# Kernel tuning notes

Hardware: AMD Instinct MI355X
Metric: run time of the kernel (lower is better)

## Reference

```python
import jax, jax.numpy as jnp
import numpy as np

C1, CS = 512, 32
EPS = 1e-5
_HI, _HJ = np.triu_indices(CS, k=1)  # pairwise (i<j) hadamard index pairs, cs_expand = 496


def setup_inputs() -> dict:
    key = jax.random.key(0)
    ks = jax.random.split(key, 9)
    B, H, W = 16, 32, 32
    return dict(
        x=jax.random.normal(ks[0], (B, C1, H, W), jnp.float32),
        fc_w=jax.random.normal(ks[1], (C1, C1), jnp.float32) * 0.05,   # 1x1 conv kernel
        fc_b=jax.random.normal(ks[2], (C1,), jnp.float32) * 0.05,
        bn_gamma=jax.random.normal(ks[3], (C1,), jnp.float32) * 0.1 + 1.0,
        bn_beta=jax.random.normal(ks[4], (C1,), jnp.float32) * 0.1,
        bn_mean=jax.random.normal(ks[5], (C1,), jnp.float32) * 0.1,    # BN running mean
        bn_var=jax.random.uniform(ks[6], (C1,), jnp.float32) + 0.5,    # BN running var (positive)
        eva_w=jax.random.normal(ks[7], (C1, C1), jnp.float32) * 0.05,
        eva_b=jax.random.normal(ks[8], (C1,), jnp.float32) * 0.05,
    )


def reference(x, fc_w, fc_b, bn_gamma, bn_beta, bn_mean, bn_var, eva_w, eva_b):
    hi = jnp.asarray(_HI)
    hj = jnp.asarray(_HJ)
    # 1x1 conv (pointwise GEMM over channels)
    x = jnp.einsum('bchw,oc->bohw', x, fc_w) + fc_b[None, :, None, None]
    # BatchNorm2d, eval mode (running stats)
    scale = bn_gamma / jnp.sqrt(bn_var + EPS)
    x = (x - bn_mean[None, :, None, None]) * scale[None, :, None, None] + bn_beta[None, :, None, None]
    # channel evaluation logits: global avg pool -> linear
    logits = jnp.mean(x, axis=(2, 3)) @ eva_w.T + eva_b  # [B, C1]
    # top-cs channel selection and gather (eval path)
    _, idx = jax.lax.top_k(logits, CS)                    # [B, CS]
    x_sel = jax.vmap(lambda xi, ii: xi[ii])(x, idx)       # [B, CS, H, W]
    # pairwise hadamard expansion: gather-multiply over (i<j) pairs
    prod = x_sel[:, hi] * x_sel[:, hj]                    # [B, cs_expand, H, W]
    # CrossHadaNorm: per-channel standardize with batch stats, affine from
    # cross-products of norm_x affine params gathered via hadamard_i/j
    mean = jnp.mean(prod, axis=(0, 2, 3), keepdims=True)
    var = jnp.var(prod, axis=(0, 2, 3), keepdims=True)
    g = (bn_gamma[hi] * bn_gamma[hj])[None, :, None, None]
    b = (bn_beta[hi] * bn_beta[hj])[None, :, None, None]
    prod = (prod - mean) / jnp.sqrt(var + EPS) * g + b
    return jnp.concatenate([x, prod], axis=1)             # [B, c1 + cs_expand, H, W]
```

## Files before the change

### kernel.cpp

```cpp
#include <hip/hip_runtime.h>
#include <stdint.h>
#include <stddef.h>

#define B_   16
#define C1_  512
#define HW_  1024
#define CS_  32
#define CE_  496
#define CO_  1008

typedef __attribute__((ext_vector_type(8))) short short8;
typedef __attribute__((ext_vector_type(4))) short short4v;
typedef __attribute__((ext_vector_type(4))) float f32x4;

__device__ __forceinline__ short f2bf(float f) {
  unsigned u = __builtin_bit_cast(unsigned, f);
  unsigned r = (u + 0x7fffu + ((u >> 16) & 1u)) >> 16;
  return (short)(unsigned short)r;
}

__device__ __forceinline__ void gload_lds16(const void* g, void* l) {
  __builtin_amdgcn_global_load_lds(
      (const __attribute__((address_space(1))) unsigned int*)g,
      (__attribute__((address_space(3))) unsigned int*)l, 16, 0, 0);
}

__global__ __launch_bounds__(256) void transpose_pool(const float* __restrict__ x,
                                                      short* __restrict__ xT,
                                                      float* __restrict__ partial,
                                                      const float* __restrict__ fc_w,
                                                      const float* __restrict__ fc_b,
                                                      const float* __restrict__ bn_gamma,
                                                      const float* __restrict__ bn_beta,
                                                      const float* __restrict__ bn_mean,
                                                      const float* __restrict__ bn_var,
                                                      short* __restrict__ wbf,
                                                      float* __restrict__ bs,
                                                      float* __restrict__ bb) {
  int bid = blockIdx.x;
  int tid = threadIdx.x;
  if (bid >= 2048) {
    if (bid < 3072) {
      int i = (bid - 2048) * 256 + tid;
      wbf[i] = f2bf(fc_w[i]);
    } else {
      for (int o = tid; o < C1_; o += 256) {
        float s = bn_gamma[o] / sqrtf(bn_var[o] + 1e-5f);
        bs[o] = s;
        bb[o] = (fc_b[o] - bn_mean[o]) * s + bn_beta[o];
      }
    }
    return;
  }
  __shared__ float tile[64][65];
  int b = bid >> 7;
  int tt = bid & 127;
  int ct = tt >> 4, pt = tt & 15;
  int c0 = ct * 64, p0 = pt * 64;
  int rr = tid >> 4, lc = tid & 15;
  const float* xb = x + (size_t)b * C1_ * HW_;
#pragma unroll
  for (int it = 0; it < 4; ++it) {
    int c = it * 16 + rr;
    int p4 = lc * 4;
    float4 v = *(const float4*)(xb + (size_t)(c0 + c) * HW_ + p0 + p4);
    tile[c][p4+0] = v.x; tile[c][p4+1] = v.y; tile[c][p4+2] = v.z; tile[c][p4+3] = v.w;
    float g = v.x + v.y + v.z + v.w;
    g += __shfl_down(g, 8, 16);
    g += __shfl_down(g, 4, 16);
    g += __shfl_down(g, 2, 16);
    g += __shfl_down(g, 1, 16);
    if (lc == 0) partial[((size_t)b * 16 + pt) * C1_ + c0 + c] = g;
  }
  __syncthreads();
#pragma unroll
  for (int it = 0; it < 4; ++it) {
    int p = it * 16 + rr;
    int c4 = lc * 4;
    short4v o;
    o[0] = f2bf(tile[c4+0][p]);
    o[1] = f2bf(tile[c4+1][p]);
    o[2] = f2bf(tile[c4+2][p]);
    o[3] = f2bf(tile[c4+3][p]);
    *(short4v*)(xT + (size_t)b * HW_ * C1_ + (size_t)(p0 + p) * C1_ + c0 + c4) = o;
  }
}

__global__ __launch_bounds__(64) void fc_pool_kernel(
    const float* __restrict__ partial, const float* __restrict__ fc_w,
    const float* __restrict__ bs, const float* __restrict__ bb,
    float* __restrict__ pb) {
  int b = blockIdx.x >> 3, ot = blockIdx.x & 7;
  int tid = threadIdx.x;
  __shared__ float px[512];
  for (int c = tid; c < 512; c += 64) {
    float s = 0.f;
#pragma unroll
    for (int pt = 0; pt < 16; ++pt) s += partial[((size_t)b * 16 + pt) * C1_ + c];
    px[c] = s * (1.f / 1024.f);
  }
  __syncthreads();
  int o = ot * 64 + tid;
  const float4* wr = (const float4*)(fc_w + (size_t)o * 512);
  float acc = 0.f;
#pragma unroll 8
  for (int q = 0; q < 128; ++q) {
    float4 w = wr[q];
    acc += w.x * px[q*4] + w.y * px[q*4+1] + w.z * px[q*4+2] + w.w * px[q*4+3];
  }
  pb[b * 512 + o] = acc * bs[o] + bb[o];
}

__global__ __launch_bounds__(64) void eva_kernel(
    const float* __restrict__ pb, const float* __restrict__ eva_w,
    const float* __restrict__ eva_b, float* __restrict__ logits) {
  int b = blockIdx.x >> 3, ot = blockIdx.x & 7;
  int tid = threadIdx.x;
  __shared__ float ps[512];
  for (int c = tid; c < 512; c += 64) ps[c] = pb[b * 512 + c];
  __syncthreads();
  int o = ot * 64 + tid;
  const float4* wr = (const float4*)(eva_w + (size_t)o * 512);
  float acc = 0.f;
#pragma unroll 8
  for (int q = 0; q < 128; ++q) {
    float4 w = wr[q];
    acc += w.x * ps[q*4] + w.y * ps[q*4+1] + w.z * ps[q*4+2] + w.w * ps[q*4+3];
  }
  logits[b * 512 + o] = acc + eva_b[o];
}

__global__ __launch_bounds__(64) void topk_kernel(const float* __restrict__ logits,
                                                  int* __restrict__ idx) {
  int b = blockIdx.x, lane = threadIdx.x;
  float v[8];
  int base = lane * 8;
#pragma unroll
  for (int u = 0; u < 8; ++u) v[u] = logits[b * 512 + base + u];
  for (int it = 0; it < CS_; ++it) {
    float bv = v[0]; int bu = 0;
#pragma unroll
    for (int u = 1; u < 8; ++u) if (v[u] > bv) { bv = v[u]; bu = u; }
    int bi = base + bu;
    for (int off = 32; off; off >>= 1) {
      float ov = __shfl_down(bv, off);
      int   oi = __shfl_down(bi, off);
      if (ov > bv || (ov == bv && oi < bi)) { bv = ov; bi = oi; }
    }
    bi = __shfl(bi, 0);
    if (lane == 0) idx[b * CS_ + it] = bi;
#pragma unroll
    for (int u = 0; u < 8; ++u) if (bi == base + u) v[u] = -3.4e38f;
  }
}

__global__ __launch_bounds__(256) void gemm_kernel(const short* __restrict__ W,
                                                   const short* __restrict__ XT,
                                                   const float* __restrict__ bs,
                                                   const float* __restrict__ bb,
                                                   float* __restrict__ out) {
  __shared__ char smem[65536];
  int bid = (blockIdx.x & 7) * 64 + (blockIdx.x >> 3);
  int b = bid >> 5;
  int t = bid & 31;
  int mt = t & 3, ntile = t >> 2;
  int m0 = mt * 128, n0 = ntile * 128;
  const short* Ag = W + (size_t)m0 * 512;
  const short* Bg = XT + (size_t)b * HW_ * 512 + (size_t)n0 * 512;
  int tid = threadIdx.x;
  int lane = tid & 63, wave = tid >> 6;
  int wr = wave >> 1, wc = wave & 1;
  int mrow = wr * 64, ncol = wc * 64;
  int lrow = lane & 15;
  int swz = (lrow & 7) << 4;

  f32x4 acc[4][4];
#pragma unroll
  for (int i = 0; i < 4; ++i)
#pragma unroll
    for (int j = 0; j < 4; ++j) acc[i][j] = (f32x4){0.f, 0.f, 0.f, 0.f};

#define STAGE(dstbase, k0)                                                      \
  {                                                                             \
    _Pragma("unroll")                                                           \
    for (int it_ = 0; it_ < 4; ++it_) {                                         \
      int s_ = it_ * 256 + tid;                                                 \
      int L_ = s_ * 16;                                                         \
      int row_ = L_ >> 7;                                                       \
      int w_ = L_ & 127;                                                        \
      int srcs_ = (w_ ^ ((row_ & 7) << 4)) >> 1;                                \
      gload_lds16(Ag + (size_t)row_ * 512 + (k0) + srcs_,                       \
                  smem + (dstbase) + L_);                                       \
      gload_lds16(Bg + (size_t)row_ * 512 + (k0) + srcs_,                       \
                  smem + 32768 + (dstbase) + L_);                               \
    }                                                                           \
  }

  STAGE(0, 0)
  asm volatile("s_waitcnt vmcnt(0)" ::: "memory");
  __syncthreads();

  int cur = 0;
  for (int kt = 0; kt < 8; ++kt) {
    if (kt < 7) STAGE((cur ^ 1) * 16384, (kt + 1) * 64)
    const char* Ab = smem + cur * 16384;
    const char* Bb = smem + 32768 + cur * 16384;
#pragma unroll
    for (int kk = 0; kk < 2; ++kk) {
      int kb = (kk * 64 + (lane >> 4) * 16) ^ swz;
      short8 af[4], bfv[4];
#pragma unroll
      for (int f = 0; f < 4; ++f) {
        af[f]  = *(const short8*)(Ab + (mrow + f * 16 + lrow) * 128 + kb);
        bfv[f] = *(const short8*)(Bb + (ncol + f * 16 + lrow) * 128 + kb);
      }
#pragma unroll
      for (int mf = 0; mf < 4; ++mf)
#pragma unroll
        for (int nf = 0; nf < 4; ++nf)
          acc[mf][nf] = __builtin_amdgcn_mfma_f32_16x16x32_bf16(af[mf], bfv[nf], acc[mf][nf], 0, 0, 0);
    }
    asm volatile("s_waitcnt vmcnt(0)" ::: "memory");
    __syncthreads();
    cur ^= 1;
  }

  float* outb = out + (size_t)b * CO_ * HW_;
#pragma unroll
  for (int mf = 0; mf < 4; ++mf) {
#pragma unroll
    for (int j = 0; j < 4; ++j) {
      int o = m0 + mrow + mf * 16 + (lane >> 4) * 4 + j;
      float s = bs[o], bv = bb[o];
#pragma unroll
      for (int nf = 0; nf < 4; ++nf) {
        int p = n0 + ncol + nf * 16 + lrow;
        outb[(size_t)o * HW_ + p] = acc[mf][nf][j] * s + bv;
      }
    }
  }
#undef STAGE
}

__global__ __launch_bounds__(256) void hada_kernel(
    const int* __restrict__ idx, const float* __restrict__ bn_gamma,
    const float* __restrict__ bn_beta, float* __restrict__ out) {
  int e = blockIdx.x, tid = threadIdx.x;
  int lane = tid & 63, wave = tid >> 6;
  int i = 0, rem = e;
  while (rem >= 31 - i) { rem -= 31 - i; ++i; }
  int j = i + 1 + rem;

  __shared__ int chi[16], chj[16];
  if (tid < 16) chi[tid] = idx[tid * CS_ + i];
  else if (tid < 32) chj[tid - 16] = idx[(tid - 16) * CS_ + j];
  __syncthreads();

  f32x4 p[16];
  float s = 0.f, s2 = 0.f;
#pragma unroll
  for (int b = 0; b < 16; ++b) {
    const float4* xi = (const float4*)(out + ((size_t)b * CO_ + chi[b]) * HW_);
    const float4* xj = (const float4*)(out + ((size_t)b * CO_ + chj[b]) * HW_);
    float4 a = xi[tid], c = xj[tid];
    p[b][0] = a.x * c.x; p[b][1] = a.y * c.y; p[b][2] = a.z * c.z; p[b][3] = a.w * c.w;
    s  += p[b][0] + p[b][1] + p[b][2] + p[b][3];
    s2 += p[b][0]*p[b][0] + p[b][1]*p[b][1] + p[b][2]*p[b][2] + p[b][3]*p[b][3];
  }
  for (int off = 32; off; off >>= 1) { s += __shfl_down(s, off); s2 += __shfl_down(s2, off); }
  __shared__ float red[8];
  if (lane == 0) { red[wave] = s; red[4 + wave] = s2; }
  __syncthreads();
  float S  = red[0] + red[1] + red[2] + red[3];
  float S2 = red[4] + red[5] + red[6] + red[7];
  float mean = S * (1.f / 16384.f);
  float var  = S2 * (1.f / 16384.f) - mean * mean;
  float sc = (bn_gamma[i] * bn_gamma[j]) / sqrtf(var + 1e-5f);
  float bi_ = bn_beta[i] * bn_beta[j] - mean * sc;

#pragma unroll
  for (int b = 0; b < 16; ++b) {
    float4 r;
    r.x = p[b][0] * sc + bi_;
    r.y = p[b][1] * sc + bi_;
    r.z = p[b][2] * sc + bi_;
    r.w = p[b][3] * sc + bi_;
    ((float4*)(out + ((size_t)b * CO_ + C1_ + e) * HW_))[tid] = r;
  }
}

#define XT_OFF     ((size_t)0)
#define WBF_OFF    ((size_t)16777216)
#define PART_OFF   ((size_t)17301504)
#define PB_OFF     ((size_t)17825792)
#define LOG_OFF    ((size_t)17858560)
#define IDX_OFF    ((size_t)17891328)
#define BS_OFF     ((size_t)17893376)
#define BB_OFF     ((size_t)17895424)

extern "C" void kernel_launch(void* const* d_in, const int* in_sizes, int n_in,
                              void* d_out, int out_size, void* d_ws, size_t ws_size,
                              hipStream_t stream) {
  const float* x        = (const float*)d_in[0];
  const float* fc_w     = (const float*)d_in[1];
  const float* fc_b     = (const float*)d_in[2];
  const float* bn_gamma = (const float*)d_in[3];
  const float* bn_beta  = (const float*)d_in[4];
  const float* bn_mean  = (const float*)d_in[5];
  const float* bn_var   = (const float*)d_in[6];
  const float* eva_w    = (const float*)d_in[7];
  const float* eva_b    = (const float*)d_in[8];
  float* out = (float*)d_out;
  char* ws = (char*)d_ws;

  short* xT      = (short*)(ws + XT_OFF);
  short* wbf     = (short*)(ws + WBF_OFF);
  float* partial = (float*)(ws + PART_OFF);
  float* pb      = (float*)(ws + PB_OFF);
  float* logits  = (float*)(ws + LOG_OFF);
  int*   idx     = (int*)(ws + IDX_OFF);
  float* bs      = (float*)(ws + BS_OFF);
  float* bb      = (float*)(ws + BB_OFF);

  hipLaunchKernelGGL(transpose_pool, dim3(3073), dim3(256), 0, stream,
                     x, xT, partial, fc_w, fc_b, bn_gamma, bn_beta, bn_mean, bn_var,
                     wbf, bs, bb);
  hipLaunchKernelGGL(fc_pool_kernel, dim3(128), dim3(64), 0, stream,
                     partial, fc_w, bs, bb, pb);
  hipLaunchKernelGGL(eva_kernel, dim3(128), dim3(64), 0, stream,
                     pb, eva_w, eva_b, logits);
  hipLaunchKernelGGL(topk_kernel, dim3(16), dim3(64), 0, stream, logits, idx);
  hipLaunchKernelGGL(gemm_kernel, dim3(512), dim3(256), 0, stream, wbf, xT, bs, bb, out);
  hipLaunchKernelGGL(hada_kernel, dim3(CE_), dim3(256), 0, stream,
                     idx, bn_gamma, bn_beta, out);
}
```

Measured before the change: 90.11 us.

## Fuse pooled-FC into GEMM launch and deepen GEMM K pipeline to four stages

The small fc_pool computation now runs in 128 extra blocks appended to the GEMM grid, which removes one kernel launch and lets it overlap with the main GEMM. The GEMM main loop changes from a double-buffered 64-wide K tile to a four-buffer, 32-wide K tile pipeline with three loads in flight. It uses partial vmcnt waits and a new XOR swizzle for the 64-byte rows. This aims to hide global-to-LDS latency better, at the cost of more barriers per K step and extra code in the GEMM kernel.

```diff
diff --git a/kernel.cpp b/kernel.cpp
--- a/kernel.cpp
+++ b/kernel.cpp
@@ -86,31 +86,6 @@
   }
 }
 
-__global__ __launch_bounds__(64) void fc_pool_kernel(
-    const float* __restrict__ partial, const float* __restrict__ fc_w,
-    const float* __restrict__ bs, const float* __restrict__ bb,
-    float* __restrict__ pb) {
-  int b = blockIdx.x >> 3, ot = blockIdx.x & 7;
-  int tid = threadIdx.x;
-  __shared__ float px[512];
-  for (int c = tid; c < 512; c += 64) {
-    float s = 0.f;
-#pragma unroll
-    for (int pt = 0; pt < 16; ++pt) s += partial[((size_t)b * 16 + pt) * C1_ + c];
-    px[c] = s * (1.f / 1024.f);
-  }
-  __syncthreads();
-  int o = ot * 64 + tid;
-  const float4* wr = (const float4*)(fc_w + (size_t)o * 512);
-  float acc = 0.f;
-#pragma unroll 8
-  for (int q = 0; q < 128; ++q) {
-    float4 w = wr[q];
-    acc += w.x * px[q*4] + w.y * px[q*4+1] + w.z * px[q*4+2] + w.w * px[q*4+3];
-  }
-  pb[b * 512 + o] = acc * bs[o] + bb[o];
-}
-
 __global__ __launch_bounds__(64) void eva_kernel(
     const float* __restrict__ pb, const float* __restrict__ eva_w,
     const float* __restrict__ eva_b, float* __restrict__ logits) {
@@ -158,8 +133,38 @@
                                                    const short* __restrict__ XT,
                                                    const float* __restrict__ bs,
                                                    const float* __restrict__ bb,
-                                                   float* __restrict__ out) {
+                                                   float* __restrict__ out,
+                                                   const float* __restrict__ partial,
+                                                   const float* __restrict__ fc_w,
+                                                   float* __restrict__ pb) {
   __shared__ char smem[65536];
+  int tid = threadIdx.x;
+
+  if (blockIdx.x >= 512) {
+    int bid2 = blockIdx.x - 512;
+    int b = bid2 >> 3, ot = bid2 & 7;
+    float* px = (float*)smem;
+    for (int c = tid; c < 512; c += 256) {
+      float s = 0.f;
+#pragma unroll
+      for (int pt = 0; pt < 16; ++pt) s += partial[((size_t)b * 16 + pt) * C1_ + c];
+      px[c] = s * (1.f / 1024.f);
+    }
+    __syncthreads();
+    if (tid < 64) {
+      int o = ot * 64 + tid;
+      const float4* wr = (const float4*)(fc_w + (size_t)o * 512);
+      float acc = 0.f;
+#pragma unroll 8
+      for (int q = 0; q < 128; ++q) {
+        float4 w = wr[q];
+        acc += w.x * px[q*4] + w.y * px[q*4+1] + w.z * px[q*4+2] + w.w * px[q*4+3];
+      }
+      pb[b * 512 + o] = acc * bs[o] + bb[o];
+    }
+    return;
+  }
+
   int bid = (blockIdx.x & 7) * 64 + (blockIdx.x >> 3);
   int b = bid >> 5;
   int t = bid & 31;
@@ -167,12 +172,11 @@
   int m0 = mt * 128, n0 = ntile * 128;
   const short* Ag = W + (size_t)m0 * 512;
   const short* Bg = XT + (size_t)b * HW_ * 512 + (size_t)n0 * 512;
-  int tid = threadIdx.x;
   int lane = tid & 63, wave = tid >> 6;
   int wr = wave >> 1, wc = wave & 1;
   int mrow = wr * 64, ncol = wc * 64;
   int lrow = lane & 15;
-  int swz = (lrow & 7) << 4;
+  int slot = lane >> 4;
 
   f32x4 acc[4][4];
 #pragma unroll
@@ -180,50 +184,52 @@
 #pragma unroll
     for (int j = 0; j < 4; ++j) acc[i][j] = (f32x4){0.f, 0.f, 0.f, 0.f};
 
-#define STAGE(dstbase, k0)                                                      \
+#define STAGE(bufidx, k0)                                                       \
   {                                                                             \
     _Pragma("unroll")                                                           \
-    for (int it_ = 0; it_ < 4; ++it_) {                                         \
+    for (int it_ = 0; it_ < 2; ++it_) {                                         \
       int s_ = it_ * 256 + tid;                                                 \
       int L_ = s_ * 16;                                                         \
-      int row_ = L_ >> 7;                                                       \
-      int w_ = L_ & 127;                                                        \
-      int srcs_ = (w_ ^ ((row_ & 7) << 4)) >> 1;                                \
-      gload_lds16(Ag + (size_t)row_ * 512 + (k0) + srcs_,                       \
-                  smem + (dstbase) + L_);                                       \
-      gload_lds16(Bg + (size_t)row_ * 512 + (k0) + srcs_,                       \
-                  smem + 32768 + (dstbase) + L_);                               \
+      int row_ = L_ >> 6;                                                       \
+      int srcb_ = (L_ & 63) ^ (((row_ >> 1) & 3) << 4);                         \
+      gload_lds16(Ag + (size_t)row_ * 512 + (k0) + (srcb_ >> 1),                \
+                  smem + (bufidx) * 8192 + L_);                                 \
+      gload_lds16(Bg + (size_t)row_ * 512 + (k0) + (srcb_ >> 1),                \
+                  smem + 32768 + (bufidx) * 8192 + L_);                         \
     }                                                                           \
   }
 
+#define STEP(KT, VN)                                                            \
+  {                                                                             \
+    asm volatile("s_waitcnt vmcnt(" #VN ")" ::: "memory");                      \
+    __builtin_amdgcn_s_barrier();                                               \
+    if ((KT) + 3 < 16) STAGE(((KT) + 3) & 3, ((KT) + 3) * 32)                   \
+    const char* Ab = smem + ((KT) & 3) * 8192;                                  \
+    const char* Bb = smem + 32768 + ((KT) & 3) * 8192;                          \
+    short8 af[4], bfv[4];                                                       \
+    _Pragma("unroll")                                                           \
+    for (int f = 0; f < 4; ++f) {                                               \
+      int rowA = mrow + f * 16 + lrow;                                          \
+      af[f] = *(const short8*)(Ab + rowA * 64 + (slot ^ ((rowA >> 1) & 3)) * 16);\
+      int rowB = ncol + f * 16 + lrow;                                          \
+      bfv[f] = *(const short8*)(Bb + rowB * 64 + (slot ^ ((rowB >> 1) & 3)) * 16);\
+    }                                                                           \
+    _Pragma("unroll")                                                           \
+    for (int mf = 0; mf < 4; ++mf)                                              \
+      _Pragma("unroll")                                                         \
+      for (int nf = 0; nf < 4; ++nf)                                            \
+        acc[mf][nf] = __builtin_amdgcn_mfma_f32_16x16x32_bf16(af[mf], bfv[nf],  \
+                                                              acc[mf][nf], 0, 0, 0); \
+  }
+
   STAGE(0, 0)
-  asm volatile("s_waitcnt vmcnt(0)" ::: "memory");
-  __syncthreads();
-
-  int cur = 0;
-  for (int kt = 0; kt < 8; ++kt) {
-    if (kt < 7) STAGE((cur ^ 1) * 16384, (kt + 1) * 64)
-    const char* Ab = smem + cur * 16384;
-    const char* Bb = smem + 32768 + cur * 16384;
-#pragma unroll
-    for (int kk = 0; kk < 2; ++kk) {
-      int kb = (kk * 64 + (lane >> 4) * 16) ^ swz;
-      short8 af[4], bfv[4];
-#pragma unroll
-      for (int f = 0; f < 4; ++f) {
-        af[f]  = *(const short8*)(Ab + (mrow + f * 16 + lrow) * 128 + kb);
-        bfv[f] = *(const short8*)(Bb + (ncol + f * 16 + lrow) * 128 + kb);
-      }
-#pragma unroll
-      for (int mf = 0; mf < 4; ++mf)
-#pragma unroll
-        for (int nf = 0; nf < 4; ++nf)
-          acc[mf][nf] = __builtin_amdgcn_mfma_f32_16x16x32_bf16(af[mf], bfv[nf], acc[mf][nf], 0, 0, 0);
-    }
-    asm volatile("s_waitcnt vmcnt(0)" ::: "memory");
-    __syncthreads();
-    cur ^= 1;
-  }
+  STAGE(1, 32)
+  STAGE(2, 64)
+
+  STEP(0, 8)  STEP(1, 8)  STEP(2, 8)  STEP(3, 8)
+  STEP(4, 8)  STEP(5, 8)  STEP(6, 8)  STEP(7, 8)
+  STEP(8, 8)  STEP(9, 8)  STEP(10, 8) STEP(11, 8)
+  STEP(12, 8) STEP(13, 8) STEP(14, 4) STEP(15, 0)
 
   float* outb = out + (size_t)b * CO_ * HW_;
 #pragma unroll
@@ -239,6 +245,7 @@
       }
     }
   }
+#undef STEP
 #undef STAGE
 }
 
@@ -325,12 +332,11 @@
   hipLaunchKernelGGL(transpose_pool, dim3(3073), dim3(256), 0, stream,
                      x, xT, partial, fc_w, fc_b, bn_gamma, bn_beta, bn_mean, bn_var,
                      wbf, bs, bb);
-  hipLaunchKernelGGL(fc_pool_kernel, dim3(128), dim3(64), 0, stream,
-                     partial, fc_w, bs, bb, pb);
+  hipLaunchKernelGGL(gemm_kernel, dim3(640), dim3(256), 0, stream,
+                     wbf, xT, bs, bb, out, partial, fc_w, pb);
   hipLaunchKernelGGL(eva_kernel, dim3(128), dim3(64), 0, stream,
                      pb, eva_w, eva_b, logits);
   hipLaunchKernelGGL(topk_kernel, dim3(16), dim3(64), 0, stream, logits, idx);
-  hipLaunchKernelGGL(gemm_kernel, dim3(512), dim3(256), 0, stream, wbf, xT, bs, bb, out);
   hipLaunchKernelGGL(hada_kernel, dim3(CE_), dim3(256), 0, stream,
                      idx, bn_gamma, bn_beta, out);
 }
```

New measurement: 83.58 us (median of 2 runs). -7.2%, faster.
